# Optimization experiments

Hardware: AMD Instinct MI355X
Metric: run time of the kernel (lower is better)

Reference implementation:

```python
import jax, jax.numpy as jnp
import numpy as np

B, S, D = 4, 4096, 64   # batch, seq_len, input_size
H, HD = 4, 16           # num_heads, head_dim


def setup_inputs() -> dict:
    key = jax.random.key(0)
    ks = jax.random.split(key, 9)
    sd = 1.0 / np.sqrt(D)          # torch Linear default uniform(-1/sqrt(fan_in), ...)
    so = 1.0 / np.sqrt(H * HD)
    u = lambda k, shape, s: jax.random.uniform(k, shape, jnp.float32, -s, s)
    return {
        "x": jax.random.normal(ks[0], (B, S, D), jnp.float32),
        "Wq": u(ks[1], (H, D, HD), sd), "bq": u(ks[2], (H, HD), sd),
        "Wk": u(ks[3], (H, D, HD), sd), "bk": u(ks[4], (H, HD), sd),
        "Wv": u(ks[5], (H, D, HD), sd), "bv": u(ks[6], (H, HD), sd),
        "Wo": u(ks[7], (H * HD, D), so), "bo": u(ks[8], (D,), so),
    }


def reference(x, Wq, bq, Wk, bk, Wv, bv, Wo, bo):
    # Batched per-head projections (fuses the original per-head Linear loop)
    q = jnp.einsum('bsd,hde->bhse', x, Wq) + bq[None, :, None, :]
    k = jnp.einsum('bsd,hde->bhse', x, Wk) + bk[None, :, None, :]
    v = jnp.einsum('bsd,hde->bhse', x, Wv) + bv[None, :, None, :]
    # scores: [B, H, S(query), S(key)]
    scores = jnp.einsum('bhse,bhte->bhst', q, k) / np.sqrt(HD).astype(np.float32)
    # FAITHFUL quirk: torch Softmax(dim=1) on [B,S,S] normalizes over the QUERY axis
    w = jax.nn.softmax(scores, axis=2)
    attended = jnp.einsum('bhst,bhte->bhse', w, v)          # [B,H,S,HD]
    concat = attended.transpose(0, 2, 1, 3).reshape(B, S, H * HD)
    out = concat @ Wo + bo                                   # [B,S,D]
    # FAITHFUL quirk: final softmax over the sequence axis (dim=1)
    return jax.nn.softmax(out, axis=1)
```

## Files before the change

kernel.cpp:

```cpp
#include <hip/hip_runtime.h>
#include <hip/hip_bf16.h>


#define BB 4
#define SS 4096
#define DD 64
#define HH 4
#define HDD 16

typedef unsigned int u32;
typedef unsigned short u16;
typedef __attribute__((ext_vector_type(8))) short bfrag;
typedef __attribute__((ext_vector_type(4))) float floatx4;
typedef __attribute__((ext_vector_type(16))) float floatx16;
typedef __attribute__((ext_vector_type(2))) u32 u32x2;
typedef __attribute__((ext_vector_type(4))) u32 u32x4;

#define LOG2E 1.4426950408889634074f
#define QSCALE (LOG2E * 0.25f)

__device__ __forceinline__ float fexp2(float x) {
#if __has_builtin(__builtin_amdgcn_exp2f)
  return __builtin_amdgcn_exp2f(x);
#else
  float r; asm("v_exp_f32 %0, %1" : "=v"(r) : "v"(x)); return r;
#endif
}
__device__ __forceinline__ float frcp(float x) {
#if __has_builtin(__builtin_amdgcn_rcpf)
  return __builtin_amdgcn_rcpf(x);
#else
  float r; asm("v_rcp_f32 %0, %1" : "=v"(r) : "v"(x)); return r;
#endif
}

__device__ __forceinline__ u16 f2bf(float f) {
  u32 u = __builtin_bit_cast(u32, f);
  return (u16)((u + 0x7FFFu + ((u >> 16) & 1u)) >> 16);
}
__device__ __forceinline__ u32 pack_bf(float lo, float hi) {
#if __has_builtin(__builtin_amdgcn_perm)
  return __builtin_amdgcn_perm(__builtin_bit_cast(u32, hi),
                               __builtin_bit_cast(u32, lo), 0x07060302u);
#else
  u32 a = __builtin_bit_cast(u32, lo);
  u32 b = __builtin_bit_cast(u32, hi);
  return (a >> 16) | (b & 0xFFFF0000u);
#endif
}

__device__ __forceinline__ void gload_lds16(const u16* g, u16* l) {
  __builtin_amdgcn_global_load_lds(
      (const __attribute__((address_space(1))) void*)(g),
      (__attribute__((address_space(3))) void*)(l), 16, 0, 0);
}

__device__ __forceinline__ int tmap(int c) {
  int c5 = c & 31;
  return (c & ~31) + (c5 & 3) + ((c5 >> 2) & 1) * 8 + ((c5 >> 3) & 1) * 16
       + ((c5 >> 4) & 1) * 4;
}

__global__ __launch_bounds__(256) void k_proj(
    const float* __restrict__ x,
    const float* __restrict__ Wq, const float* __restrict__ bq,
    const float* __restrict__ Wk, const float* __restrict__ bk,
    const float* __restrict__ Wv, const float* __restrict__ bv,
    u16* __restrict__ qb, u16* __restrict__ kb, float* __restrict__ vf)
{
  __shared__ float xs[16 * 64];
  const int tid = threadIdx.x;
  const int blk = blockIdx.x;
  const int b   = blk >> 8;
  const int s0  = (blk & 255) << 4;
  ((float4*)xs)[tid] = ((const float4*)(x + ((size_t)b * SS + s0) * DD))[tid];
  __syncthreads();

  const int col = tid & 63, h = col >> 4, e = col & 15;
  const int rg  = tid >> 6;
  float aq[4] = {0,0,0,0}, ak[4] = {0,0,0,0}, av[4] = {0,0,0,0};
  const int wofs = h * (DD * HDD) + e;
#pragma unroll 4
  for (int d = 0; d < DD; ++d) {
    float wq = Wq[wofs + d * HDD];
    float wk = Wk[wofs + d * HDD];
    float wv = Wv[wofs + d * HDD];
    const float* xr = xs + (rg * 4) * 64 + d;
#pragma unroll
    for (int r = 0; r < 4; ++r) {
      float xv = xr[r * 64];
      aq[r] += xv * wq; ak[r] += xv * wk; av[r] += xv * wv;
    }
  }
  const float bqv = bq[col], bkv = bk[col], bvv = bv[col];
  size_t base = ((size_t)(b * HH + h) * SS + (s0 + rg * 4)) * HDD + e;
#pragma unroll
  for (int r = 0; r < 4; ++r) {
    qb[base + r * HDD] = f2bf((aq[r] + bqv) * QSCALE);
    kb[base + r * HDD] = f2bf(ak[r] + bkv);
    vf[base + r * HDD] = av[r] + bvv;
  }
}

__global__ __launch_bounds__(256, 4) void k_colsum(
    const u16* __restrict__ qb, const u16* __restrict__ kb,
    float* __restrict__ csp)
{
  const int tid = threadIdx.x;
  const int lane = tid & 63, w = tid >> 6;
  const int l31 = lane & 31, hl = lane >> 5;
  const int bh = blockIdx.z, chunk = blockIdx.y;
  const int t0 = blockIdx.x * 128 + w * 32;
  const size_t base = (size_t)bh * (SS * HDD);

  const bfrag kf = *(const bfrag*)(kb + base + (size_t)(t0 + l31) * HDD + hl * 8);
  const u16* qp = qb + base + ((size_t)chunk * 1024 + l31) * HDD + hl * 8;
  const floatx16 z16 = {0.f};
  float c0 = 0.f, c1 = 0.f, c2 = 0.f, c3 = 0.f;

#define LQ(i) (*(const bfrag*)(qp + (size_t)((i) * 32) * HDD))
#define ACCUM(dv)                                   \
  do {                                              \
    _Pragma("unroll")                               \
    for (int j = 0; j < 4; ++j) {                   \
      c0 += fexp2((dv)[4 * j + 0]);                 \
      c1 += fexp2((dv)[4 * j + 1]);                 \
      c2 += fexp2((dv)[4 * j + 2]);                 \
      c3 += fexp2((dv)[4 * j + 3]);                 \
    }                                               \
  } while (0)

  bfrag q0 = LQ(0), q1 = LQ(1), q2v = LQ(2), q3 = LQ(3);
#pragma unroll
  for (int i = 0; i < 32; i += 4) {
    {
      floatx16 d = __builtin_amdgcn_mfma_f32_32x32x16_bf16(q0, kf, z16, 0, 0, 0);
      if (i + 4 < 32) q0 = LQ(i + 4);
      ACCUM(d);
    }
    {
      floatx16 d = __builtin_amdgcn_mfma_f32_32x32x16_bf16(q1, kf, z16, 0, 0, 0);
      if (i + 5 < 32) q1 = LQ(i + 5);
      ACCUM(d);
    }
    {
      floatx16 d = __builtin_amdgcn_mfma_f32_32x32x16_bf16(q2v, kf, z16, 0, 0, 0);
      if (i + 6 < 32) q2v = LQ(i + 6);
      ACCUM(d);
    }
    {
      floatx16 d = __builtin_amdgcn_mfma_f32_32x32x16_bf16(q3, kf, z16, 0, 0, 0);
      if (i + 7 < 32) q3 = LQ(i + 7);
      ACCUM(d);
    }
  }
#undef LQ
#undef ACCUM

  float c = (c0 + c1) + (c2 + c3);
  c += __shfl_xor(c, 32, 64);
  if (hl == 0)
    csp[((size_t)bh * 4 + chunk) * SS + t0 + l31] = c;
}

__global__ __launch_bounds__(256) void k_vprep(
    const float* __restrict__ vf, const float* __restrict__ csp,
    u16* __restrict__ vp)
{
  __shared__ float vstage[256 * 16];
  __shared__ float rcls[256];
  const int tid = threadIdx.x;
  const int chunk = blockIdx.x;
  const int bh = blockIdx.y;
  const int t0 = chunk << 8;
  {
    const float4* src = (const float4*)(vf + ((size_t)bh * SS + t0) * HDD);
    float4* dst = (float4*)vstage;
#pragma unroll
    for (int i = 0; i < 4; ++i) dst[tid + 256 * i] = src[tid + 256 * i];
    const float* cp = csp + (size_t)bh * 4 * SS + t0 + tid;
    rcls[tid] = frcp(cp[0] + cp[SS] + cp[2 * SS] + cp[3 * SS]);
  }
  __syncthreads();
  u16* outb = vp + ((size_t)bh * 16 + chunk) * 4096;
#pragma unroll
  for (int gi = 0; gi < 2; ++gi) {
    const int g = gi * 256 + tid;
    const int e = g >> 5, gg = g & 31;
    const int cbase = (gg ^ (e & 7)) << 3;
    u32 r[4];
#pragma unroll
    for (int jj = 0; jj < 4; ++jj) {
      int ta = tmap(cbase + 2 * jj);
      int tb = tmap(cbase + 2 * jj + 1);
      u16 lo = f2bf(vstage[ta * 16 + e] * rcls[ta]);
      u16 hi = f2bf(vstage[tb * 16 + e] * rcls[tb]);
      r[jj] = (u32)lo | ((u32)hi << 16);
    }
    u32x4 vv = {r[0], r[1], r[2], r[3]};
    *(u32x4*)(outb + g * 8) = vv;
  }
}

__global__ __launch_bounds__(256, 4) void k_attn(
    const u16* __restrict__ qb, const u16* __restrict__ kb,
    const u16* __restrict__ vp, float* __restrict__ attp)
{
  __shared__ __align__(16) u16 vls[2][4096];
  const int tid  = threadIdx.x;
  const int lane = tid & 63, w = tid >> 6;
  const int l31 = lane & 31, hl = lane >> 5;
  const int bh = blockIdx.z, b = bh >> 2, h = bh & 3;
  const int tph = blockIdx.y;
  const int s0 = blockIdx.x * 128 + w * 32;
  const size_t base = (size_t)bh * (SS * HDD);

  const bfrag qf = *(const bfrag*)(qb + base + (size_t)(s0 + l31) * HDD + hl * 8);
  const u16* kp = kb + base + ((size_t)tph * 2048 + l31) * HDD + hl * 8;
  const floatx16 z16 = {0.f};
  floatx16 acc = {0.f};

  const u16* vsrc = vp + ((size_t)bh * 16 + tph * 8) * 4096;

  {
    const u16* gs = vsrc + w * 1024 + lane * 8;
    u16* ls = &vls[0][0] + w * 1024;
    gload_lds16(gs, ls);
    gload_lds16(gs + 512, ls + 512);
  }
  bfrag kfr[8];
#pragma unroll
  for (int it = 0; it < 8; ++it)
    kfr[it] = *(const bfrag*)(kp + (size_t)(it * 32) * HDD);
  __syncthreads();

#pragma unroll
  for (int ch = 0; ch < 8; ++ch) {
    if (ch < 7) {
      const u16* gs = vsrc + (ch + 1) * 4096 + w * 1024 + lane * 8;
      u16* ls = &vls[(ch + 1) & 1][0] + w * 1024;
      gload_lds16(gs, ls);
      gload_lds16(gs + 512, ls + 512);
    }

    const u16* vrow = &vls[ch & 1][0] + (l31 & 15) * 256;
    const int eb = l31 & 7;
#pragma unroll
    for (int it = 0; it < 8; ++it) {
      bfrag kf = kfr[it];
      if (ch < 7)
        kfr[it] = *(const bfrag*)(kp + (size_t)((ch + 1) * 256 + it * 32) * HDD);
      floatx16 d = __builtin_amdgcn_mfma_f32_32x32x16_bf16(kf, qf, z16, 0, 0, 0);
      u32 wr[8];
#pragma unroll
      for (int p = 0; p < 8; ++p)
        wr[p] = pack_bf(fexp2(d[2 * p]), fexp2(d[2 * p + 1]));
      const int cc0 = it * 4 + hl * 2;
      u32x4 af0 = *(const u32x4*)(vrow + ((cc0 ^ eb) << 3));
      u32x4 af1 = *(const u32x4*)(vrow + (((cc0 + 1) ^ eb) << 3));
      u32x4 ef0 = {wr[0], wr[1], wr[2], wr[3]};
      u32x4 ef1 = {wr[4], wr[5], wr[6], wr[7]};
      acc = __builtin_amdgcn_mfma_f32_32x32x16_bf16(
          __builtin_bit_cast(bfrag, af0), __builtin_bit_cast(bfrag, ef0), acc, 0, 0, 0);
      acc = __builtin_amdgcn_mfma_f32_32x32x16_bf16(
          __builtin_bit_cast(bfrag, af1), __builtin_bit_cast(bfrag, ef1), acc, 0, 0, 0);
    }
    __syncthreads();
  }

  float* ao = attp + (((size_t)tph * BB + b) * SS + s0 + l31) * (HH * HDD)
            + h * HDD + 4 * hl;
  float4 lo4 = {acc[0], acc[1], acc[2], acc[3]};
  float4 hi4 = {acc[4], acc[5], acc[6], acc[7]};
  *(float4*)ao       = lo4;
  *(float4*)(ao + 8) = hi4;
}

__global__ __launch_bounds__(256) void k_oproj(
    const float* __restrict__ att, const float* __restrict__ Wo,
    const float* __restrict__ bo, float* __restrict__ outp,
    float* __restrict__ part)
{
  __shared__ float wols[64 * 64];
  __shared__ float red[4][64];
  const int tid = threadIdx.x;
  const int blk = blockIdx.x;
  const int b = blk >> 9, s0 = (blk & 511) << 3;
#pragma unroll
  for (int i = 0; i < 4; ++i)
    ((float4*)wols)[tid + 256 * i] = ((const float4*)Wo)[tid + 256 * i];
  __syncthreads();

  const int d = tid & 63, sg = tid >> 6;
  const float bov = bo[d];
  const size_t so = (size_t)BB * SS * 16;
  float es = 0.f;
#pragma unroll
  for (int r = 0; r < 2; ++r) {
    int s = s0 + sg * 2 + r;
    const floatx4* row = (const floatx4*)(att + ((size_t)b * SS + s) * 64);
    float acc = bov;
#pragma unroll
    for (int j = 0; j < 16; ++j) {
      floatx4 c = row[j] + row[j + so];
      acc += c[0] * wols[(4*j+0)*64 + d] + c[1] * wols[(4*j+1)*64 + d]
           + c[2] * wols[(4*j+2)*64 + d] + c[3] * wols[(4*j+3)*64 + d];
    }
    outp[((size_t)b * SS + s) * 64 + d] = acc;
    es += fexp2(acc * LOG2E);
  }
  red[sg][d] = es;
  __syncthreads();
  if (tid < 64)
    part[((size_t)b * 512 + (blk & 511)) * 64 + tid] =
        red[0][tid] + red[1][tid] + red[2][tid] + red[3][tid];
}

__global__ __launch_bounds__(256) void k_softmax(
    const float* __restrict__ outp, const float* __restrict__ part,
    float* __restrict__ out)
{
  __shared__ float red[4][64];
  __shared__ float rs[64];
  const int tid = threadIdx.x, d = tid & 63, sg = tid >> 6;
  const int st = blockIdx.x;
  const int b = blockIdx.y;
  {
    float e = 0.f;
    const float* pp = part + ((size_t)b * 512 + sg * 128) * 64 + d;
#pragma unroll 8
    for (int c = 0; c < 128; ++c) e += pp[c * 64];
    red[sg][d] = e;
  }
  __syncthreads();
  if (tid < 64)
    rs[tid] = frcp(red[0][tid] + red[1][tid] + red[2][tid] + red[3][tid]);
  __syncthreads();
  const float r = rs[d];
  const size_t rowbase = ((size_t)b * SS + st * 64 + sg * 16) * 64 + d;
#pragma unroll 4
  for (int i = 0; i < 16; ++i)
    out[rowbase + i * 64] = fexp2(outp[rowbase + i * 64] * LOG2E) * r;
}

extern "C" void kernel_launch(void* const* d_in, const int* in_sizes, int n_in,
                              void* d_out, int out_size, void* d_ws, size_t ws_size,
                              hipStream_t stream) {
  const float* x  = (const float*)d_in[0];
  const float* Wq = (const float*)d_in[1];
  const float* bq = (const float*)d_in[2];
  const float* Wk = (const float*)d_in[3];
  const float* bk = (const float*)d_in[4];
  const float* Wv = (const float*)d_in[5];
  const float* bv = (const float*)d_in[6];
  const float* Wo = (const float*)d_in[7];
  const float* bo = (const float*)d_in[8];

  char* ws = (char*)d_ws;
  constexpr size_t QB_OFF  = 0;
  constexpr size_t KB_OFF  = (size_t)2  << 20;
  constexpr size_t VF_OFF  = (size_t)4  << 20;
  constexpr size_t CSP_OFF = (size_t)8  << 20;
  constexpr size_t VP_OFF  = (size_t)9  << 20;
  constexpr size_t ATT_OFF = (size_t)11 << 20;
  constexpr size_t OUT_OFF = (size_t)19 << 20;
  constexpr size_t PT_OFF  = (size_t)23 << 20;

  u16*   qb   = (u16*)  (ws + QB_OFF);
  u16*   kb   = (u16*)  (ws + KB_OFF);
  float* vf   = (float*)(ws + VF_OFF);
  float* csp  = (float*)(ws + CSP_OFF);
  u16*   vpb  = (u16*)  (ws + VP_OFF);
  float* attp = (float*)(ws + ATT_OFF);
  float* outp = (float*)(ws + OUT_OFF);
  float* part = (float*)(ws + PT_OFF);
  float* out  = (float*)d_out;

  hipLaunchKernelGGL(k_proj,    dim3(1024),       dim3(256), 0, stream,
                     x, Wq, bq, Wk, bk, Wv, bv, qb, kb, vf);
  hipLaunchKernelGGL(k_colsum,  dim3(32, 4, 16),  dim3(256), 0, stream, qb, kb, csp);
  hipLaunchKernelGGL(k_vprep,   dim3(16, 16),     dim3(256), 0, stream, vf, csp, vpb);
  hipLaunchKernelGGL(k_attn,    dim3(32, 2, 16),  dim3(256), 0, stream,
                     qb, kb, vpb, attp);
  hipLaunchKernelGGL(k_oproj,   dim3(2048),       dim3(256), 0, stream,
                     attp, Wo, bo, outp, part);
  hipLaunchKernelGGL(k_softmax, dim3(64, 4),      dim3(256), 0, stream, outp, part, out);
}
```

Measured before the change: 182.0 us.

## Fuse column-sum and V-prep kernels, looping each block over all query chunks

The separate column-sum and V-normalisation kernels are merged into one. Each block now loops over the full query range for its 128 keys, so the complete softmax denominator stays on-chip. The reciprocal is kept in shared memory and used to scale and repack V to bf16 right away. This removes a kernel launch and the global round trip of the partial column sums. In exchange the grid shrinks fourfold (fewer, longer blocks), which lowers parallelism during the exp-heavy phase. The prefetch also reads past the end of the Q slice on the last iteration.

```diff
diff --git a/kernel.cpp b/kernel.cpp
--- a/kernel.cpp
+++ b/kernel.cpp
@@ -102,23 +102,32 @@
   }
 }
 
-__global__ __launch_bounds__(256, 4) void k_colsum(
+__global__ __launch_bounds__(256, 4) void k_csvp(
     const u16* __restrict__ qb, const u16* __restrict__ kb,
-    float* __restrict__ csp)
-{
+    const float* __restrict__ vf, u16* __restrict__ vp)
+{
+  __shared__ float vstage[128 * 16];
+  __shared__ float rcl[128];
   const int tid = threadIdx.x;
   const int lane = tid & 63, w = tid >> 6;
   const int l31 = lane & 31, hl = lane >> 5;
-  const int bh = blockIdx.z, chunk = blockIdx.y;
-  const int t0 = blockIdx.x * 128 + w * 32;
+  const int bx = blockIdx.x;
+  const int bh = blockIdx.y;
+  const int t0 = bx * 128 + w * 32;
   const size_t base = (size_t)bh * (SS * HDD);
 
+  {
+    const float4* vsrc4 = (const float4*)(vf + ((size_t)bh * SS + bx * 128) * HDD);
+    ((float4*)vstage)[tid]       = vsrc4[tid];
+    ((float4*)vstage)[tid + 256] = vsrc4[tid + 256];
+  }
+
   const bfrag kf = *(const bfrag*)(kb + base + (size_t)(t0 + l31) * HDD + hl * 8);
-  const u16* qp = qb + base + ((size_t)chunk * 1024 + l31) * HDD + hl * 8;
+  const u16* qpc = qb + base + (size_t)l31 * HDD + hl * 8;
   const floatx16 z16 = {0.f};
   float c0 = 0.f, c1 = 0.f, c2 = 0.f, c3 = 0.f;
 
-#define LQ(i) (*(const bfrag*)(qp + (size_t)((i) * 32) * HDD))
+#define LQ(i) (*(const bfrag*)(qpc + (size_t)(i) * (32 * HDD)))
 #define ACCUM(dv)                                   \
   do {                                              \
     _Pragma("unroll")                               \
@@ -131,28 +140,28 @@
   } while (0)
 
   bfrag q0 = LQ(0), q1 = LQ(1), q2v = LQ(2), q3 = LQ(3);
-#pragma unroll
-  for (int i = 0; i < 32; i += 4) {
-    {
-      floatx16 d = __builtin_amdgcn_mfma_f32_32x32x16_bf16(q0, kf, z16, 0, 0, 0);
-      if (i + 4 < 32) q0 = LQ(i + 4);
-      ACCUM(d);
-    }
-    {
-      floatx16 d = __builtin_amdgcn_mfma_f32_32x32x16_bf16(q1, kf, z16, 0, 0, 0);
-      if (i + 5 < 32) q1 = LQ(i + 5);
-      ACCUM(d);
-    }
-    {
-      floatx16 d = __builtin_amdgcn_mfma_f32_32x32x16_bf16(q2v, kf, z16, 0, 0, 0);
-      if (i + 6 < 32) q2v = LQ(i + 6);
-      ACCUM(d);
-    }
-    {
-      floatx16 d = __builtin_amdgcn_mfma_f32_32x32x16_bf16(q3, kf, z16, 0, 0, 0);
-      if (i + 7 < 32) q3 = LQ(i + 7);
-      ACCUM(d);
-    }
+#pragma unroll 1
+  for (int o = 0; o < 4; ++o) {
+#pragma unroll
+    for (int i = 0; i < 32; i += 4) {
+      {
+        floatx16 d = __builtin_amdgcn_mfma_f32_32x32x16_bf16(q0, kf, z16, 0, 0, 0);
+        q0 = LQ(i + 4);  ACCUM(d);
+      }
+      {
+        floatx16 d = __builtin_amdgcn_mfma_f32_32x32x16_bf16(q1, kf, z16, 0, 0, 0);
+        q1 = LQ(i + 5);  ACCUM(d);
+      }
+      {
+        floatx16 d = __builtin_amdgcn_mfma_f32_32x32x16_bf16(q2v, kf, z16, 0, 0, 0);
+        q2v = LQ(i + 6); ACCUM(d);
+      }
+      {
+        floatx16 d = __builtin_amdgcn_mfma_f32_32x32x16_bf16(q3, kf, z16, 0, 0, 0);
+        q3 = LQ(i + 7);  ACCUM(d);
+      }
+    }
+    qpc += 32 * 32 * HDD;
   }
 #undef LQ
 #undef ACCUM
@@ -160,46 +169,26 @@
   float c = (c0 + c1) + (c2 + c3);
   c += __shfl_xor(c, 32, 64);
   if (hl == 0)
-    csp[((size_t)bh * 4 + chunk) * SS + t0 + l31] = c;
-}
-
-__global__ __launch_bounds__(256) void k_vprep(
-    const float* __restrict__ vf, const float* __restrict__ csp,
-    u16* __restrict__ vp)
-{
-  __shared__ float vstage[256 * 16];
-  __shared__ float rcls[256];
-  const int tid = threadIdx.x;
-  const int chunk = blockIdx.x;
-  const int bh = blockIdx.y;
-  const int t0 = chunk << 8;
-  {
-    const float4* src = (const float4*)(vf + ((size_t)bh * SS + t0) * HDD);
-    float4* dst = (float4*)vstage;
-#pragma unroll
-    for (int i = 0; i < 4; ++i) dst[tid + 256 * i] = src[tid + 256 * i];
-    const float* cp = csp + (size_t)bh * 4 * SS + t0 + tid;
-    rcls[tid] = frcp(cp[0] + cp[SS] + cp[2 * SS] + cp[3 * SS]);
-  }
-  __syncthreads();
-  u16* outb = vp + ((size_t)bh * 16 + chunk) * 4096;
-#pragma unroll
-  for (int gi = 0; gi < 2; ++gi) {
-    const int g = gi * 256 + tid;
-    const int e = g >> 5, gg = g & 31;
-    const int cbase = (gg ^ (e & 7)) << 3;
-    u32 r[4];
-#pragma unroll
-    for (int jj = 0; jj < 4; ++jj) {
-      int ta = tmap(cbase + 2 * jj);
-      int tb = tmap(cbase + 2 * jj + 1);
-      u16 lo = f2bf(vstage[ta * 16 + e] * rcls[ta]);
-      u16 hi = f2bf(vstage[tb * 16 + e] * rcls[tb]);
-      r[jj] = (u32)lo | ((u32)hi << 16);
-    }
-    u32x4 vv = {r[0], r[1], r[2], r[3]};
-    *(u32x4*)(outb + g * 8) = vv;
-  }
+    rcl[w * 32 + l31] = frcp(c);
+  __syncthreads();
+
+  const int e = tid >> 4;
+  const int h0 = bx & 1;
+  const int poff = h0 * 16 + (tid & 15);
+  const int cc = poff ^ (e & 7);
+  const int h128 = h0 * 128;
+  u32 r[4];
+#pragma unroll
+  for (int jj = 0; jj < 4; ++jj) {
+    int ta = tmap(cc * 8 + 2 * jj)     - h128;
+    int tb = tmap(cc * 8 + 2 * jj + 1) - h128;
+    u16 lo = f2bf(vstage[ta * 16 + e] * rcl[ta]);
+    u16 hi = f2bf(vstage[tb * 16 + e] * rcl[tb]);
+    r[jj] = (u32)lo | ((u32)hi << 16);
+  }
+  u16* outb = vp + ((size_t)bh * 16 + (bx >> 1)) * 4096;
+  u32x4 vv = {r[0], r[1], r[2], r[3]};
+  *(u32x4*)(outb + e * 256 + poff * 8) = vv;
 }
 
 __global__ __launch_bounds__(256, 4) void k_attn(
@@ -360,16 +349,14 @@
   constexpr size_t QB_OFF  = 0;
   constexpr size_t KB_OFF  = (size_t)2  << 20;
   constexpr size_t VF_OFF  = (size_t)4  << 20;
-  constexpr size_t CSP_OFF = (size_t)8  << 20;
-  constexpr size_t VP_OFF  = (size_t)9  << 20;
-  constexpr size_t ATT_OFF = (size_t)11 << 20;
-  constexpr size_t OUT_OFF = (size_t)19 << 20;
-  constexpr size_t PT_OFF  = (size_t)23 << 20;
+  constexpr size_t VP_OFF  = (size_t)8  << 20;
+  constexpr size_t ATT_OFF = (size_t)10 << 20;
+  constexpr size_t OUT_OFF = (size_t)18 << 20;
+  constexpr size_t PT_OFF  = (size_t)22 << 20;
 
   u16*   qb   = (u16*)  (ws + QB_OFF);
   u16*   kb   = (u16*)  (ws + KB_OFF);
   float* vf   = (float*)(ws + VF_OFF);
-  float* csp  = (float*)(ws + CSP_OFF);
   u16*   vpb  = (u16*)  (ws + VP_OFF);
   float* attp = (float*)(ws + ATT_OFF);
   float* outp = (float*)(ws + OUT_OFF);
@@ -378,8 +365,8 @@
 
   hipLaunchKernelGGL(k_proj,    dim3(1024),       dim3(256), 0, stream,
                      x, Wq, bq, Wk, bk, Wv, bv, qb, kb, vf);
-  hipLaunchKernelGGL(k_colsum,  dim3(32, 4, 16),  dim3(256), 0, stream, qb, kb, csp);
-  hipLaunchKernelGGL(k_vprep,   dim3(16, 16),     dim3(256), 0, stream, vf, csp, vpb);
+  hipLaunchKernelGGL(k_csvp,    dim3(32, 16),     dim3(256), 0, stream,
+                     qb, kb, vf, vpb);
   hipLaunchKernelGGL(k_attn,    dim3(32, 2, 16),  dim3(256), 0, stream,
                      qb, kb, vpb, attp);
   hipLaunchKernelGGL(k_oproj,   dim3(2048),       dim3(256), 0, stream,
```

Measured after the change: 184.7 us. Within noise of the previous version (+1.5%).
